# Performance work log

Hardware: AMD Instinct MI355X
Metric: run time of the kernel (lower is better)

## Reference

```python
import jax, jax.numpy as jnp
import numpy as np
import math

N_EMBD = 1024
NUM_HEADS = 16
MAX_LEN = 2048
AUX = 256
B, T = 2, 2048


def setup_inputs() -> dict:
    key = jax.random.key(0)
    ks = jax.random.split(key, 16)
    s = 0.02
    C, A = N_EMBD, AUX
    inp = {
        "x": jax.random.normal(ks[0], (B, T, C), jnp.float32),
        "aux_x": jax.random.normal(ks[1], (B, T, A), jnp.float32),
        "Wq": s * jax.random.normal(ks[2], (C, C), jnp.float32),
        "bq": jnp.zeros((C,), jnp.float32),
        "Wk": s * jax.random.normal(ks[3], (C + A, C), jnp.float32),
        "bk": jnp.zeros((C,), jnp.float32),
        "Wv": s * jax.random.normal(ks[4], (C + A, C), jnp.float32),
        "bv": jnp.zeros((C,), jnp.float32),
        "Wo": s * jax.random.normal(ks[5], (C, C), jnp.float32),  # zero-init in source; randomized for a meaningful baseline
        "bo": jnp.zeros((C,), jnp.float32),
        "PEq": s * jax.random.normal(ks[6], (MAX_LEN, C), jnp.float32),
        "PEk": s * jax.random.normal(ks[7], (MAX_LEN, C), jnp.float32),
        "attn_mask": jax.random.bernoulli(ks[8], 0.9, (B, T, T)),
        "frame_indices": jax.random.randint(ks[9], (B, T), 0, MAX_LEN),
        "num_heads": NUM_HEADS,
    }
    return inp


def reference(x, aux_x, Wq, bq, Wk, bk, Wv, bv, Wo, bo, PEq, PEk, attn_mask, frame_indices, num_heads):
    Bx, Tx, C = x.shape
    H = num_heads
    hd = C // H
    x_aug = jnp.concatenate([x, aux_x], axis=2)  # [B,T,C+A]
    # QKV projections, split heads; PE added per (position, head) to q and k
    q = (x @ Wq + bq).reshape(Bx, Tx, H, hd) + PEq[frame_indices].reshape(Bx, Tx, H, hd)
    k = (x_aug @ Wk + bk).reshape(Bx, Tx, H, hd) + PEk[frame_indices].reshape(Bx, Tx, H, hd)
    v = (x_aug @ Wv + bv).reshape(Bx, Tx, H, hd)
    scale = 1.0 / math.sqrt(hd)
    scores = jnp.einsum("bqhd,bkhd->bhqk", q, k) * scale  # [B,H,T,T]
    scores = jnp.where(attn_mask[:, None, :, :], scores, -jnp.inf)
    attn = jax.nn.softmax(scores, axis=-1)  # fully-masked rows -> NaN
    out = jnp.einsum("bhqk,bkhd->bqhd", attn, v).reshape(Bx, Tx, C)
    out = jnp.nan_to_num(out, nan=0.0)
    return out @ Wo + bo
```

## Files before the change

kernel.cpp:

```cpp
#include <hip/hip_runtime.h>
#include <hip/hip_bf16.h>

typedef unsigned short u16;
typedef unsigned int u32;
typedef __attribute__((ext_vector_type(8))) short bf16x8;
typedef __attribute__((ext_vector_type(4))) float f32x4;

#define HD 64
#define NH 16
#define TT 2048
#define BB 2
#define CA 1280

__device__ __forceinline__ u16 bfu(float f) {
    u32 u = __builtin_bit_cast(u32, f);
    u32 r = u + 0x7fffu + ((u >> 16) & 1u);
    return (u16)(r >> 16);
}

__device__ __forceinline__ float ex2(float x) {
#if __has_builtin(__builtin_amdgcn_exp2f)
    return __builtin_amdgcn_exp2f(x);
#else
    return exp2f(x);
#endif
}

__device__ __forceinline__ void gload16(const void* g, void* l) {
    __builtin_amdgcn_global_load_lds(
        (const __attribute__((address_space(1))) unsigned int*)g,
        (__attribute__((address_space(3))) unsigned int*)l,
        16, 0, 0);
}

__global__ void prep(const float* __restrict__ x, const float* __restrict__ aux,
                     u16* __restrict__ xa,
                     const float* __restrict__ Wq, const float* __restrict__ Wk,
                     const float* __restrict__ Wv, const float* __restrict__ Wo,
                     u16* __restrict__ WTall, u16* __restrict__ WTo,
                     const unsigned char* __restrict__ m, u32* __restrict__ bits) {
    int bid = blockIdx.x;
    if (bid < 5120) {
        int i = bid * 256 + threadIdx.x;
        int row = i / 320;
        int c4 = i - row * 320;
        float4 v;
        if (c4 < 256) v = ((const float4*)x)[row * 256 + c4];
        else          v = ((const float4*)aux)[row * 64 + (c4 - 256)];
        ushort4 pk; pk.x = bfu(v.x); pk.y = bfu(v.y); pk.z = bfu(v.z); pk.w = bfu(v.w);
        ((ushort4*)xa)[i] = pk;
    } else if (bid < 10240) {
        int t = bid - 5120;
        int z = t / 1280;
        int inner = t - z * 1280;
        int kt = (inner % 40) * 32;
        int nt = (inner / 40) * 32;
        const float* src = (z == 0) ? Wq : (z == 1) ? Wk : (z == 2) ? Wv : Wo;
        u16* dst = (z == 3) ? WTo : WTall + (size_t)z * 1024 * 1280;
        int Ksrc = (z == 0 || z == 3) ? 1024 : 1280;
        int Kpad = (z == 3) ? 1024 : 1280;
        if (kt >= Kpad) return;
        __shared__ float tile[32][33];
        int r = threadIdx.x >> 5, c = threadIdx.x & 31;
        #pragma unroll
        for (int i = 0; i < 4; i++) {
            int k = kt + r + i * 8;
            tile[r + i * 8][c] = (k < Ksrc) ? src[(size_t)k * 1024 + nt + c] : 0.f;
        }
        __syncthreads();
        #pragma unroll
        for (int i = 0; i < 4; i++) {
            int n = nt + r + i * 8;
            dst[(size_t)n * Kpad + kt + c] = bfu(tile[c][r + i * 8]);
        }
    } else {
        __shared__ u32 modeSh;
        if (threadIdx.x == 0) modeSh = 0;
        __syncthreads();
        const u32* wp = (const u32*)m;
        u32 local = 0;
        for (int j = threadIdx.x; j < 2048; j += 256) {
            u32 v = wp[j];
            if (v == 0x3f800000u) local |= 2u;
            else if (v > 1u) local |= 1u;
            if ((j & 1) && v != 0u) local |= 4u;
        }
        if (local) atomicOr(&modeSh, local);
        __syncthreads();
        u32 mode = modeSh;
        bool words32 = (mode & 2u) || (mode == 4u);
        bool bytes8 = !words32 && (mode & 1u);

        int i = (bid - 10240) * 256 + threadIdx.x;
        size_t e0 = (size_t)i * 32;
        u32 r = 0;
        if (words32) {
            const uint4* q = (const uint4*)(wp + e0);
            #pragma unroll
            for (int j4 = 0; j4 < 8; j4++) {
                uint4 v = q[j4];
                if (v.x) r |= 1u << (j4 * 4 + 0);
                if (v.y) r |= 1u << (j4 * 4 + 1);
                if (v.z) r |= 1u << (j4 * 4 + 2);
                if (v.w) r |= 1u << (j4 * 4 + 3);
            }
        } else if (bytes8) {
            const unsigned char* p = m + e0;
            uint4 a = *(const uint4*)p;
            uint4 b = *(const uint4*)(p + 16);
            u32 words[8] = {a.x, a.y, a.z, a.w, b.x, b.y, b.z, b.w};
            #pragma unroll
            for (int jw = 0; jw < 8; jw++) {
                u32 xw = words[jw];
                r |= ((xw >> 0) & 1u) << (jw * 4 + 0);
                r |= ((xw >> 8) & 1u) << (jw * 4 + 1);
                r |= ((xw >> 16) & 1u) << (jw * 4 + 2);
                r |= ((xw >> 24) & 1u) << (jw * 4 + 3);
            }
        } else {
            #pragma unroll 4
            for (int j = 0; j < 32; j++)
                if (wp[(e0 + j) * 2]) r |= 1u << j;
        }
        bits[i] = r;
    }
}

template <int MODE>
__global__ __launch_bounds__(256, 3) void gemm_bt(
    const u16* __restrict__ A, const u16* __restrict__ Bt, int K,
    const float* __restrict__ biasq, const float* __restrict__ biask,
    const float* __restrict__ biasv, const float* __restrict__ PEq,
    const float* __restrict__ PEk, const int* __restrict__ fidx,
    u16* __restrict__ qo, u16* __restrict__ ko, u16* __restrict__ vto,
    float* __restrict__ fo, const float* __restrict__ bo) {
    __shared__ u16 As[128 * 64];
    __shared__ u16 Bs[128 * 64];
    const int tid = threadIdx.x, lane = tid & 63, w = tid >> 6;
    const int l15 = lane & 15, l4 = lane >> 4;
    const int wm = w >> 1, wn = w & 1;
    int bm, bn;
    if (MODE == 0) {
        int bid = blockIdx.x;
        bm = (bid & 7) * 4 + ((bid >> 3) & 3);
        bn = bid >> 5;
    } else {
        bm = blockIdx.x; bn = blockIdx.y;
    }
    const int Keff = (MODE == 0 && (bn >> 3) == 0) ? 1024 : K;

    f32x4 acc[4][4] = {};

    const int srow = lane >> 3;
    const int schunk = (lane & 7) ^ srow;
    const u16* ag = A + (size_t)(bm * 128 + w * 32 + srow) * K + schunk * 8;
    const u16* bg = Bt + (size_t)(bn * 128 + w * 32 + srow) * K + schunk * 8;
    u16* asl = &As[(w * 32) * 64] + lane * 8;
    u16* bsl = &Bs[(w * 32) * 64] + lane * 8;

    for (int kt = 0; kt < Keff; kt += 64) {
        #pragma unroll
        for (int i = 0; i < 4; i++) {
            gload16(ag + (size_t)i * 8 * K + kt, asl + i * 8 * 64);
            gload16(bg + (size_t)i * 8 * K + kt, bsl + i * 8 * 64);
        }
        __syncthreads();
        #pragma unroll
        for (int ks = 0; ks < 2; ks++) {
            bf16x8 af[4], bfr[4];
            #pragma unroll
            for (int mi = 0; mi < 4; mi++) {
                int row = wm * 64 + mi * 16 + l15;
                af[mi] = *(const bf16x8*)&As[row * 64 + (((ks * 4 + l4) ^ (row & 7)) * 8)];
            }
            #pragma unroll
            for (int ni = 0; ni < 4; ni++) {
                int row = wn * 64 + ni * 16 + l15;
                bfr[ni] = *(const bf16x8*)&Bs[row * 64 + (((ks * 4 + l4) ^ (row & 7)) * 8)];
            }
            #pragma unroll
            for (int mi = 0; mi < 4; mi++)
                #pragma unroll
                for (int ni = 0; ni < 4; ni++)
                    acc[mi][ni] = __builtin_amdgcn_mfma_f32_16x16x32_bf16(
                        af[mi], bfr[ni], acc[mi][ni], 0, 0, 0);
        }
        __syncthreads();
    }

    if (MODE == 0) {
        int sec = bn >> 3;
        if (sec < 2) {
            const float* bias = sec ? biask : biasq;
            const float* PE   = sec ? PEk : PEq;
            u16* outp = sec ? ko : qo;
            float scl = sec ? 1.0f : 0.180336880111120419f;
            #pragma unroll
            for (int mi = 0; mi < 4; mi++) {
                #pragma unroll
                for (int r = 0; r < 4; r++) {
                    int m = bm * 128 + wm * 64 + mi * 16 + l4 * 4 + r;
                    int b = m >> 11, t = m & 2047;
                    int fi = fidx[m];
                    #pragma unroll
                    for (int ni = 0; ni < 4; ni++) {
                        int nn = (bn & 7) * 128 + wn * 64 + ni * 16 + l15;
                        float val = (acc[mi][ni][r] + bias[nn] + PE[(size_t)fi * 1024 + nn]) * scl;
                        outp[((size_t)(b * NH + (nn >> 6)) * TT + t) * HD + (nn & 63)] = bfu(val);
                    }
                }
            }
        } else {
            int b = bm >> 4;
            int t0 = (bm & 15) * 128 + wm * 64;
            #pragma unroll
            for (int ni = 0; ni < 4; ni++) {
                int nn = (bn - 16) * 128 + wn * 64 + ni * 16 + l15;
                float bvv = biasv[nn];
                int h = nn >> 6, d = nn & 63;
                u16* dst = vto + ((size_t)((b * NH + h) * HD + d)) * TT + t0;
                #pragma unroll
                for (int mi = 0; mi < 4; mi++) {
                    ushort4 pk;
                    pk.x = bfu(acc[mi][ni][0] + bvv);
                    pk.y = bfu(acc[mi][ni][1] + bvv);
                    pk.z = bfu(acc[mi][ni][2] + bvv);
                    pk.w = bfu(acc[mi][ni][3] + bvv);
                    *(ushort4*)(dst + mi * 16 + l4 * 4) = pk;
                }
            }
        }
    } else {
        #pragma unroll
        for (int mi = 0; mi < 4; mi++) {
            #pragma unroll
            for (int r = 0; r < 4; r++) {
                int m = bm * 128 + wm * 64 + mi * 16 + l4 * 4 + r;
                #pragma unroll
                for (int ni = 0; ni < 4; ni++) {
                    int ng = bn * 128 + wn * 64 + ni * 16 + l15;
                    fo[(size_t)m * 1024 + ng] = acc[mi][ni][r] + bo[ng];
                }
            }
        }
    }
}

__global__ __launch_bounds__(256, 2) void attn_fwd(
    const u16* __restrict__ Q, const u16* __restrict__ Kg,
    const u16* __restrict__ VT, const u32* __restrict__ mbits,
    u16* __restrict__ Og) {
    __shared__ u16 KPs[128 * 136];
    __shared__ u16 Vs[64 * 128];
    const int tid = threadIdx.x, lane = tid & 63, w = tid >> 6;
    const int l15 = lane & 15, l4 = lane >> 4;
    const int s_ = blockIdx.x;
    const int qt = (s_ >> 3) & 15;
    const int bh = (s_ & 7) * 4 + (s_ >> 7);
    const int b = bh >> 4;
    const size_t hoff = (size_t)bh * (TT * HD);

    bf16x8 qf[2][2];
    #pragma unroll
    for (int mi = 0; mi < 2; mi++)
        #pragma unroll
        for (int ks = 0; ks < 2; ks++)
            qf[mi][ks] = *(const bf16x8*)&Q[hoff +
                (size_t)(qt * 128 + w * 32 + mi * 16 + l15) * HD + ks * 32 + l4 * 8];

    bf16x8 ones;
    #pragma unroll
    for (int j = 0; j < 8; j++) ones[j] = (short)0x3F80;

    f32x4 po[2][4] = {};
    f32x4 pol[2] = {};

    const int srow = lane >> 3;
    const int schunk = (lane & 7) ^ srow;
    const u16* kgl = Kg + hoff + (size_t)(w * 32 + srow) * HD + schunk * 8;
    u16* ksl = &KPs[(w * 32) * 64] + lane * 8;
    const size_t voff = (size_t)bh * (HD * TT);
    const size_t mbase = ((size_t)(b * TT + qt * 128 + w * 32 + l4 * 4)) * 64;
    const int shEven = 31 - l15, shOdd = 15 - l15;

    for (int kt = 0; kt < 16; kt++) {
        uint4 mb[2][4];
        #pragma unroll
        for (int mi = 0; mi < 2; mi++)
            #pragma unroll
            for (int r = 0; r < 4; r++)
                mb[mi][r] = *(const uint4*)&mbits[mbase + (size_t)(mi * 16 + r) * 64 + kt * 4];

        #pragma unroll
        for (int i = 0; i < 4; i++)
            gload16(kgl + (size_t)(kt * 128 + i * 8) * HD, ksl + i * 8 * 64);
        #pragma unroll
        for (int i = 0; i < 4; i++) {
            int d = w * 16 + i * 4 + l4;
            const u16* src = VT + voff + (size_t)d * TT + kt * 128 + ((l15 ^ (d & 15)) * 8);
            gload16(src, &Vs[(w * 16 + i * 4) * 128] + lane * 8);
        }
        __syncthreads();

        f32x4 s[2][8];
        __builtin_amdgcn_s_setprio(1);
        #pragma unroll
        for (int nt = 0; nt < 8; nt++) {
            int krow = nt * 16 + l15;
            bf16x8 kf0 = *(const bf16x8*)&KPs[krow * 64 + (((0 + l4) ^ (krow & 7)) * 8)];
            bf16x8 kf1 = *(const bf16x8*)&KPs[krow * 64 + (((4 + l4) ^ (krow & 7)) * 8)];
            #pragma unroll
            for (int mi = 0; mi < 2; mi++) {
                f32x4 z = {0.f, 0.f, 0.f, 0.f};
                z = __builtin_amdgcn_mfma_f32_16x16x32_bf16(qf[mi][0], kf0, z, 0, 0, 0);
                s[mi][nt] = __builtin_amdgcn_mfma_f32_16x16x32_bf16(qf[mi][1], kf1, z, 0, 0, 0);
            }
        }
        __builtin_amdgcn_s_setprio(0);
        __syncthreads();

        #pragma unroll
        for (int mi = 0; mi < 2; mi++) {
            #pragma unroll
            for (int r = 0; r < 4; r++) {
                u32 mw[4] = {mb[mi][r].x, mb[mi][r].y, mb[mi][r].z, mb[mi][r].w};
                int prow = w * 32 + mi * 16 + l4 * 4 + r;
                u16* pw = &KPs[prow * 136 + l15];
                #pragma unroll
                for (int nt = 0; nt < 8; nt++) {
                    u32 word = mw[nt >> 1];
                    int sh = (nt & 1) ? shOdd : shEven;
                    u32 ext = (u32)(((int)(word << sh)) >> 31);
                    float p = ex2(s[mi][nt][r]);
                    u32 pb = __builtin_bit_cast(u32, p) & ext;
                    pw[nt * 16] = (u16)(pb >> 16);
                }
            }
        }

        bf16x8 pf[2][4];
        #pragma unroll
        for (int mi = 0; mi < 2; mi++)
            #pragma unroll
            for (int ks = 0; ks < 4; ks++)
                pf[mi][ks] = *(const bf16x8*)&KPs[(w * 32 + mi * 16 + l15) * 136 + ks * 32 + l4 * 8];
        __builtin_amdgcn_s_setprio(1);
        #pragma unroll
        for (int nto = 0; nto < 4; nto++) {
            #pragma unroll
            for (int ks = 0; ks < 4; ks++) {
                int d = nto * 16 + l15;
                bf16x8 vf = *(const bf16x8*)&Vs[d * 128 + (((ks * 4 + l4) ^ (d & 15)) * 8)];
                #pragma unroll
                for (int mi = 0; mi < 2; mi++)
                    po[mi][nto] = __builtin_amdgcn_mfma_f32_16x16x32_bf16(
                        pf[mi][ks], vf, po[mi][nto], 0, 0, 0);
            }
        }
        #pragma unroll
        for (int mi = 0; mi < 2; mi++)
            #pragma unroll
            for (int ks = 0; ks < 4; ks++)
                pol[mi] = __builtin_amdgcn_mfma_f32_16x16x32_bf16(pf[mi][ks], ones, pol[mi], 0, 0, 0);
        __builtin_amdgcn_s_setprio(0);
        __syncthreads();
    }

    int h = bh & 15;
    #pragma unroll
    for (int mi = 0; mi < 2; mi++) {
        #pragma unroll
        for (int r = 0; r < 4; r++) {
            float lv = pol[mi][r];
            float inv = (lv > 0.f) ? (1.f / lv) : 0.f;
            int t = qt * 128 + w * 32 + mi * 16 + l4 * 4 + r;
            #pragma unroll
            for (int nto = 0; nto < 4; nto++)
                Og[((size_t)(b * TT + t)) * 1024 + h * 64 + nto * 16 + l15] =
                    bfu(po[mi][nto][r] * inv);
        }
    }
}

extern "C" void kernel_launch(void* const* d_in, const int* in_sizes, int n_in,
                              void* d_out, int out_size, void* d_ws, size_t ws_size,
                              hipStream_t stream) {
    const float* x   = (const float*)d_in[0];
    const float* aux = (const float*)d_in[1];
    const float* Wq  = (const float*)d_in[2];
    const float* bq  = (const float*)d_in[3];
    const float* Wk  = (const float*)d_in[4];
    const float* bk  = (const float*)d_in[5];
    const float* Wv  = (const float*)d_in[6];
    const float* bv  = (const float*)d_in[7];
    const float* Wo  = (const float*)d_in[8];
    const float* bo  = (const float*)d_in[9];
    const float* PEq = (const float*)d_in[10];
    const float* PEk = (const float*)d_in[11];
    const unsigned char* mask = (const unsigned char*)d_in[12];
    const int* fidx  = (const int*)d_in[13];
    float* out = (float*)d_out;

    char* ws = (char*)d_ws;
    u16* XA    = (u16*)(ws + 0);
    u16* AttO  = (u16*)(ws + 0);
    u16* WTall = (u16*)(ws + 10485760);
    u16* WTo   = (u16*)(ws + 18350080);
    u16* Qb    = (u16*)(ws + 20447232);
    u16* Kb    = (u16*)(ws + 28835840);
    u16* VTb   = (u16*)(ws + 45613056);
    u32* MB    = (u32*)(ws + 54001664);

    prep<<<11264, 256, 0, stream>>>(x, aux, XA, Wq, Wk, Wv, Wo, WTall, WTo, mask, MB);

    gemm_bt<0><<<768, 256, 0, stream>>>(
        XA, WTall, 1280, bq, bk, bv, PEq, PEk, fidx, Qb, Kb, VTb, nullptr, nullptr);

    attn_fwd<<<512, 256, 0, stream>>>(Qb, Kb, VTb, MB, AttO);

    gemm_bt<1><<<dim3(32, 8), 256, 0, stream>>>(
        AttO, WTo, 1024, nullptr, nullptr, nullptr, nullptr, nullptr, nullptr,
        nullptr, nullptr, nullptr, out, bo);
}
```

Measured before the change: 142.1 us.

## Double-buffer K/V tiles in attention with 64-key blocks and separate P buffer

The attention kernel now works on 64-key tiles instead of 128 and keeps two LDS buffers for K and V. The next tile's global loads are issued before computing on the current one, which hides load latency and removes one barrier per iteration. P gets its own LDS buffer instead of reusing the K buffer. In exchange the loop runs twice as many iterations, each with a barrier and less MFMA work, and the double-buffer prefetch relies on the async gload16 having completed by the single end-of-iteration sync.

```diff
diff --git a/kernel.cpp b/kernel.cpp
--- a/kernel.cpp
+++ b/kernel.cpp
@@ -250,8 +250,9 @@
     const u16* __restrict__ Q, const u16* __restrict__ Kg,
     const u16* __restrict__ VT, const u32* __restrict__ mbits,
     u16* __restrict__ Og) {
-    __shared__ u16 KPs[128 * 136];
-    __shared__ u16 Vs[64 * 128];
+    __shared__ u16 Ks[2][64 * 64];
+    __shared__ u16 Vs[2][64 * 64];
+    __shared__ u16 Ps[128 * 72];
     const int tid = threadIdx.x, lane = tid & 63, w = tid >> 6;
     const int l15 = lane & 15, l4 = lane >> 4;
     const int s_ = blockIdx.x;
@@ -277,38 +278,42 @@
 
     const int srow = lane >> 3;
     const int schunk = (lane & 7) ^ srow;
-    const u16* kgl = Kg + hoff + (size_t)(w * 32 + srow) * HD + schunk * 8;
-    u16* ksl = &KPs[(w * 32) * 64] + lane * 8;
-    const size_t voff = (size_t)bh * (HD * TT);
+    const u16* kgl = Kg + hoff + (size_t)(w * 16 + srow) * HD + schunk * 8;
+    const u16* vgl = VT + (size_t)bh * (HD * TT) + (size_t)(w * 16 + srow) * TT + schunk * 8;
+    const int ldst = (w * 16) * 64 + lane * 8;
     const size_t mbase = ((size_t)(b * TT + qt * 128 + w * 32 + l4 * 4)) * 64;
     const int shEven = 31 - l15, shOdd = 15 - l15;
 
-    for (int kt = 0; kt < 16; kt++) {
-        uint4 mb[2][4];
+    #pragma unroll
+    for (int i = 0; i < 2; i++) {
+        gload16(kgl + (size_t)(i * 8) * HD, &Ks[0][ldst + i * 8 * 64]);
+        gload16(vgl + (size_t)(i * 8) * TT, &Vs[0][ldst + i * 8 * 64]);
+    }
+    __syncthreads();
+
+    for (int kt = 0; kt < 32; kt++) {
+        const int cur = kt & 1;
+        if (kt < 31) {
+            #pragma unroll
+            for (int i = 0; i < 2; i++) {
+                gload16(kgl + (size_t)((kt + 1) * 64 + i * 8) * HD, &Ks[cur ^ 1][ldst + i * 8 * 64]);
+                gload16(vgl + (size_t)(i * 8) * TT + (kt + 1) * 64, &Vs[cur ^ 1][ldst + i * 8 * 64]);
+            }
+        }
+        uint2 mb[2][4];
         #pragma unroll
         for (int mi = 0; mi < 2; mi++)
             #pragma unroll
             for (int r = 0; r < 4; r++)
-                mb[mi][r] = *(const uint4*)&mbits[mbase + (size_t)(mi * 16 + r) * 64 + kt * 4];
-
-        #pragma unroll
-        for (int i = 0; i < 4; i++)
-            gload16(kgl + (size_t)(kt * 128 + i * 8) * HD, ksl + i * 8 * 64);
-        #pragma unroll
-        for (int i = 0; i < 4; i++) {
-            int d = w * 16 + i * 4 + l4;
-            const u16* src = VT + voff + (size_t)d * TT + kt * 128 + ((l15 ^ (d & 15)) * 8);
-            gload16(src, &Vs[(w * 16 + i * 4) * 128] + lane * 8);
-        }
-        __syncthreads();
-
-        f32x4 s[2][8];
+                mb[mi][r] = *(const uint2*)&mbits[mbase + (size_t)(mi * 16 + r) * 64 + kt * 2];
+
+        f32x4 s[2][4];
         __builtin_amdgcn_s_setprio(1);
         #pragma unroll
-        for (int nt = 0; nt < 8; nt++) {
+        for (int nt = 0; nt < 4; nt++) {
             int krow = nt * 16 + l15;
-            bf16x8 kf0 = *(const bf16x8*)&KPs[krow * 64 + (((0 + l4) ^ (krow & 7)) * 8)];
-            bf16x8 kf1 = *(const bf16x8*)&KPs[krow * 64 + (((4 + l4) ^ (krow & 7)) * 8)];
+            bf16x8 kf0 = *(const bf16x8*)&Ks[cur][krow * 64 + (((0 + l4) ^ (krow & 7)) * 8)];
+            bf16x8 kf1 = *(const bf16x8*)&Ks[cur][krow * 64 + (((4 + l4) ^ (krow & 7)) * 8)];
             #pragma unroll
             for (int mi = 0; mi < 2; mi++) {
                 f32x4 z = {0.f, 0.f, 0.f, 0.f};
@@ -317,17 +322,16 @@
             }
         }
         __builtin_amdgcn_s_setprio(0);
-        __syncthreads();
 
         #pragma unroll
         for (int mi = 0; mi < 2; mi++) {
             #pragma unroll
             for (int r = 0; r < 4; r++) {
-                u32 mw[4] = {mb[mi][r].x, mb[mi][r].y, mb[mi][r].z, mb[mi][r].w};
+                u32 mw[2] = {mb[mi][r].x, mb[mi][r].y};
                 int prow = w * 32 + mi * 16 + l4 * 4 + r;
-                u16* pw = &KPs[prow * 136 + l15];
-                #pragma unroll
-                for (int nt = 0; nt < 8; nt++) {
+                u16* pw = &Ps[prow * 72 + l15];
+                #pragma unroll
+                for (int nt = 0; nt < 4; nt++) {
                     u32 word = mw[nt >> 1];
                     int sh = (nt & 1) ? shOdd : shEven;
                     u32 ext = (u32)(((int)(word << sh)) >> 31);
@@ -338,19 +342,19 @@
             }
         }
 
-        bf16x8 pf[2][4];
+        bf16x8 pf[2][2];
         #pragma unroll
         for (int mi = 0; mi < 2; mi++)
             #pragma unroll
-            for (int ks = 0; ks < 4; ks++)
-                pf[mi][ks] = *(const bf16x8*)&KPs[(w * 32 + mi * 16 + l15) * 136 + ks * 32 + l4 * 8];
+            for (int ks = 0; ks < 2; ks++)
+                pf[mi][ks] = *(const bf16x8*)&Ps[(w * 32 + mi * 16 + l15) * 72 + ks * 32 + l4 * 8];
         __builtin_amdgcn_s_setprio(1);
         #pragma unroll
         for (int nto = 0; nto < 4; nto++) {
             #pragma unroll
-            for (int ks = 0; ks < 4; ks++) {
+            for (int ks = 0; ks < 2; ks++) {
                 int d = nto * 16 + l15;
-                bf16x8 vf = *(const bf16x8*)&Vs[d * 128 + (((ks * 4 + l4) ^ (d & 15)) * 8)];
+                bf16x8 vf = *(const bf16x8*)&Vs[cur][d * 64 + (((ks * 4 + l4) ^ (d & 7)) * 8)];
                 #pragma unroll
                 for (int mi = 0; mi < 2; mi++)
                     po[mi][nto] = __builtin_amdgcn_mfma_f32_16x16x32_bf16(
@@ -360,7 +364,7 @@
         #pragma unroll
         for (int mi = 0; mi < 2; mi++)
             #pragma unroll
-            for (int ks = 0; ks < 4; ks++)
+            for (int ks = 0; ks < 2; ks++)
                 pol[mi] = __builtin_amdgcn_mfma_f32_16x16x32_bf16(pf[mi][ks], ones, pol[mi], 0, 0, 0);
         __builtin_amdgcn_s_setprio(0);
         __syncthreads();
```

Result: slower. 145.7 us (+2.6%).
